# Kernel optimization log

Hardware: AMD Instinct MI355X
Metric: run time of the kernel (lower is better)

The kernel has to match this reference:

```python
import jax, jax.numpy as jnp
import numpy as np

B, C_IN, IMG = 4, 1, 256
E, P = 800, 4            # embed_size, patch_size
H, DH, M = 8, 64, 64     # heads, dim_head=heads**2, num_landmarks
N = (IMG // P) ** 2      # 4096 tokens
OUT = 256                # output_size
RESK = 33                # lucidrains residual depthwise conv kernel
BN_EPS = 1e-5
LN_EPS = 1e-5
PINV_ITERS = 6


def setup_inputs() -> dict:
    key = jax.random.key(0)
    ks = iter(jax.random.split(key, 32))
    def nrm(shape, s=0.02):
        return jax.random.normal(next(ks), shape, jnp.float32) * s
    inp = {"x": jax.random.normal(next(ks), (B, C_IN, IMG, IMG), jnp.float32)}
    # conv stack: (in, out, kernel); last conv has stride=P, padding=0
    for i, (ci, co, kk) in enumerate([(C_IN, 64, 3), (64, 128, 3), (128, 256, 3), (256, E, P)]):
        inp[f"w{i}"] = nrm((co, ci, kk, kk), 0.05)
        inp[f"b{i}"] = jnp.zeros((co,), jnp.float32)
        inp[f"g{i}"] = jnp.ones((co,), jnp.float32)    # BN gamma
        inp[f"be{i}"] = jnp.zeros((co,), jnp.float32)  # BN beta
        inp[f"mu{i}"] = nrm((co,), 0.1)                # BN running mean
        inp[f"var{i}"] = jax.random.uniform(next(ks), (co,), jnp.float32, 0.5, 1.5)
    inp["qkv_w"] = nrm((E, 3 * H * DH))      # to_qkv (no bias)
    inp["out_w"] = nrm((H * DH, E))          # to_out linear
    inp["out_b"] = jnp.zeros((E,), jnp.float32)
    inp["res_w"] = nrm((H, 1, RESK, 1), 0.05)  # depthwise residual conv over token dim
    inp["ln_g"] = jnp.ones((E,), jnp.float32)
    inp["ln_b"] = jnp.zeros((E,), jnp.float32)
    inp["head_w"] = nrm((E, OUT * OUT // N))   # Linear(800, 16)
    inp["head_b"] = jnp.zeros((OUT * OUT // N,), jnp.float32)
    return inp


def conv2d(x, w, b, stride, pad):
    y = jax.lax.conv_general_dilated(x, w, (stride, stride), [(pad, pad), (pad, pad)],
                                     dimension_numbers=("NCHW", "OIHW", "NCHW"))
    return y + b[None, :, None, None]


def bn(x, g, be, mu, var):
    s = g * jax.lax.rsqrt(var + BN_EPS)  # eval-mode BatchNorm
    return x * s[None, :, None, None] + (be - mu * s)[None, :, None, None]


def moore_penrose_pinv(a, iters=PINV_ITERS):
    I = jnp.eye(a.shape[-1], dtype=a.dtype)
    z = jnp.swapaxes(a, -1, -2) / (jnp.max(jnp.abs(a).sum(-1)) * jnp.max(jnp.abs(a).sum(-2)))
    for _ in range(iters):
        az = a @ z
        z = 0.25 * z @ (13.0 * I - az @ (15.0 * I - az @ (7.0 * I - az)))
    return z


def reference(x, w0, b0, g0, be0, mu0, var0, w1, b1, g1, be1, mu1, var1,
              w2, b2, g2, be2, mu2, var2, w3, b3, g3, be3, mu3, var3,
              qkv_w, out_w, out_b, res_w, ln_g, ln_b, head_w, head_b):
    # ---- PatchEmbedConv ----
    h = x
    blocks = [(w0, b0, g0, be0, mu0, var0, 1, 1), (w1, b1, g1, be1, mu1, var1, 1, 1),
              (w2, b2, g2, be2, mu2, var2, 1, 1), (w3, b3, g3, be3, mu3, var3, P, 0)]
    for w, b, g, be, mu, var, st, pd in blocks:
        h = jax.nn.relu(bn(conv2d(h, w, b, st, pd), g, be, mu, var))
    tok = h.reshape(B, E, N).transpose(0, 2, 1)  # [B, N, E]

    # ---- NystromAttention (n % m == 0, so no front padding needed) ----
    qkv = tok @ qkv_w  # [B, N, 3*H*DH]
    q, k, v = [t.reshape(B, N, H, DH).transpose(0, 2, 1, 3) for t in jnp.split(qkv, 3, axis=-1)]
    q = q * (DH ** -0.5)
    l = N // M
    q_l = q.reshape(B, H, M, l, DH).mean(3)  # landmark means over consecutive blocks
    k_l = k.reshape(B, H, M, l, DH).mean(3)
    a1 = jax.nn.softmax(jnp.einsum("bhnd,bhmd->bhnm", q, k_l), axis=-1)    # [B,H,N,M]
    a2 = jax.nn.softmax(jnp.einsum("bhmd,bhkd->bhmk", q_l, k_l), axis=-1)  # [B,H,M,M]
    a3 = jax.nn.softmax(jnp.einsum("bhmd,bhnd->bhmn", q_l, k), axis=-1)    # [B,H,M,N]
    out = (a1 @ moore_penrose_pinv(a2)) @ (a3 @ v)  # [B,H,N,DH]
    # residual depthwise conv over the token dim of v (groups = heads)
    res = jax.lax.conv_general_dilated(v, res_w, (1, 1), [(RESK // 2, RESK // 2), (0, 0)],
                                       dimension_numbers=("NCHW", "OIHW", "NCHW"),
                                       feature_group_count=H)
    out = out + res
    out = out.transpose(0, 2, 1, 3).reshape(B, N, H * DH)
    out = out @ out_w + out_b  # [B, N, E]

    # ---- LayerNorm ----
    mu_t = out.mean(-1, keepdims=True)
    var_t = out.var(-1, keepdims=True)
    out = (out - mu_t) * jax.lax.rsqrt(var_t + LN_EPS) * ln_g + ln_b

    # ---- reconstruction head ----
    y = jax.nn.sigmoid(out @ head_w + head_b)  # [B, N, OUT*OUT/N]
    return y.reshape(-1, 1, OUT, OUT)
```

## Files before the change

kernel.cpp:

```cpp
#include <hip/hip_runtime.h>

#define DI __device__ __forceinline__

constexpr float BN_EPS_C = 1e-5f;
constexpr float LN_EPS_C = 1e-5f;

typedef _Float16 half8 __attribute__((ext_vector_type(8)));
typedef float f32x4 __attribute__((ext_vector_type(4)));

constexpr size_t B_H0   = 0;
constexpr size_t B_H1   = 8388608;
constexpr size_t B_H2   = 25165824;
constexpr size_t B_Q    = 25165824;
constexpr size_t B_V    = 58720256;
constexpr size_t B_KT   = 75497472;
constexpr size_t B_ATT  = 92274688;
constexpr size_t B_LNB  = 25165824;
constexpr size_t B_TOK  = 159383552;
constexpr size_t B_WP1  = 185597952;
constexpr size_t B_WP2  = 185745408;
constexpr size_t B_WP3  = 186335232;
constexpr size_t B_QKVT = 192888832;
constexpr size_t B_OWT  = 195346432;
constexpr size_t B_QL   = 196165632;
constexpr size_t B_KL   = 196689920;
constexpr size_t B_KLH  = 197214208;
constexpr size_t B_A2   = 197476352;
constexpr size_t B_W2T  = 198524928;
constexpr size_t B_A3V  = 198787072;
constexpr size_t B_SCAL = 199311360;
constexpr size_t B_HWH  = 199311424;

DI float blockReduceSum(float v) {
  #pragma unroll
  for (int o = 32; o; o >>= 1) v += __shfl_xor(v, o);
  __shared__ float red[4];
  int w = threadIdx.x >> 6;
  __syncthreads();
  if ((threadIdx.x & 63) == 0) red[w] = v;
  __syncthreads();
  return red[0] + red[1] + red[2] + red[3];
}

template <int LP, int RP>
DI void mm16(const float* L, const float* R, int r0, int c0, float reg[4][4]) {
  #pragma unroll
  for (int i = 0; i < 4; ++i)
    #pragma unroll
    for (int j = 0; j < 4; ++j) reg[i][j] = 0.f;
  for (int dd = 0; dd < 64; ++dd) {
    float l[4], r[4];
    #pragma unroll
    for (int i = 0; i < 4; ++i) l[i] = L[(size_t)(r0 + i) * LP + dd];
    #pragma unroll
    for (int j = 0; j < 4; ++j) r[j] = R[(size_t)dd * RP + c0 + j];
    #pragma unroll
    for (int i = 0; i < 4; ++i)
      #pragma unroll
      for (int j = 0; j < 4; ++j) reg[i][j] = fmaf(l[i], r[j], reg[i][j]);
  }
}

__global__ void k_pack_all(
    const float* __restrict__ w1, const float* __restrict__ w2c, const float* __restrict__ w3,
    const float* __restrict__ qkvw, const float* __restrict__ outw, const float* __restrict__ headw,
    _Float16* __restrict__ wp1, _Float16* __restrict__ wp2, _Float16* __restrict__ wp3,
    _Float16* __restrict__ qkvT, _Float16* __restrict__ owT, _Float16* __restrict__ hwh,
    float* __restrict__ scal) {
  size_t i = (size_t)blockIdx.x * 256 + threadIdx.x;
  if (i < 73728) {
    int q = i % 9, ci = (i / 9) % 64, co = i / (9 * 64);
    wp1[((size_t)co * 9 + q) * 64 + ci] = (_Float16)w1[i];
  } else if (i < 368640) {
    size_t j = i - 73728;
    int q = j % 9, ci = (j / 9) % 128, co = j / (9 * 128);
    wp2[((size_t)co * 9 + q) * 128 + ci] = (_Float16)w2c[j];
  } else if (i < 3645440) {
    size_t j = i - 368640;
    int q = j % 16, ci = (j / 16) % 256, co = j / (16 * 256);
    wp3[((size_t)co * 16 + q) * 256 + ci] = (_Float16)w3[j];
  } else if (i < 4874240) {
    size_t j = i - 3645440;
    int n = j % 1536, k = j / 1536;
    qkvT[(size_t)n * 800 + k] = (_Float16)qkvw[j];
  } else if (i < 5283840) {
    size_t j = i - 4874240;
    int n = j % 800, k = j / 800;
    owT[(size_t)n * 512 + k] = (_Float16)outw[j];
  } else if (i < 5296640) {
    size_t j = i - 5283840;
    int n = j % 16, k = j / 16;
    hwh[(size_t)n * 800 + k] = (_Float16)headw[j];
  } else if (i < 5296642) {
    scal[i - 5296640] = 0.f;
  }
}

__global__ __launch_bounds__(256) void k_conv0(
    const float* __restrict__ xb, const float* __restrict__ w0, const float* __restrict__ b0,
    const float* __restrict__ g0, const float* __restrict__ be0, const float* __restrict__ mu0,
    const float* __restrict__ var0, _Float16* __restrict__ h0) {
  const int t = threadIdx.x, co = t & 63, xg = t >> 6;
  const int y = blockIdx.x;
  float wreg[9];
  #pragma unroll
  for (int q = 0; q < 9; ++q) wreg[q] = w0[co * 9 + q];
  float s = g0[co] * rsqrtf(var0[co] + BN_EPS_C);
  float sh = fmaf(b0[co] - mu0[co], s, be0[co]);
  for (int xl = 0; xl < 64; ++xl) {
    int xx = xg * 64 + xl;
    float acc = 0.f;
    #pragma unroll
    for (int dy = 0; dy < 3; ++dy) {
      int yy = y + dy - 1;
      if ((unsigned)yy >= 256u) continue;
      #pragma unroll
      for (int dx = 0; dx < 3; ++dx) {
        int xi = xx + dx - 1;
        if ((unsigned)xi >= 256u) continue;
        acc = fmaf(wreg[dy * 3 + dx], xb[yy * 256 + xi], acc);
      }
    }
    float v = fmaxf(fmaf(acc, s, sh), 0.f);
    h0[((size_t)y * 256 + xx) * 64 + co] = (_Float16)v;
  }
}

template <int CI>
__global__ __launch_bounds__(256) void k_convs(
    const _Float16* __restrict__ in, const _Float16* __restrict__ wp,
    const float* __restrict__ bias, const float* __restrict__ g, const float* __restrict__ be,
    const float* __restrict__ mu, const float* __restrict__ var,
    _Float16* __restrict__ out, int CO, int NCT) {
  __shared__ _Float16 Ab[2][128 * 40];
  __shared__ _Float16 Bb[2][128 * 40];
  constexpr int CPQ = CI / 32;
  constexpr int NCK = 9 * CPQ;
  const int t = threadIdx.x;
  const int bid = blockIdx.x;
  const int xcd = bid & 7, slot = bid >> 3;
  const int pj = slot / NCT, cc = slot % NCT;
  const int p = pj * 8 + xcd;
  const int r0 = p * 128, c0 = cc * 128;

  const int ma = t >> 2, kga = t & 3;
  int ry[2], rx[2];
  #pragma unroll
  for (int s = 0; s < 2; ++s) {
    int r = r0 + ma + s * 64;
    ry[s] = r >> 8;
    rx[s] = r & 255;
  }
  const _Float16* baseB[2];
  #pragma unroll
  for (int s = 0; s < 2; ++s)
    baseB[s] = wp + (size_t)(c0 + ma + s * 64) * 9 * CI + kga * 8;
  const int wo = ma * 40 + kga * 8;

  auto loadA = [&](int s, int ck) -> half8 {
    int q = ck / CPQ, coff = (ck % CPQ) * 32;
    int yy = ry[s] + q / 3 - 1;
    int xx = rx[s] + q % 3 - 1;
    half8 a = {};
    if ((unsigned)yy < 256u && (unsigned)xx < 256u)
      a = *reinterpret_cast<const half8*>(in + ((size_t)yy * 256 + xx) * CI + coff + kga * 8);
    return a;
  };

  {
    half8 a0 = loadA(0, 0), a1 = loadA(1, 0);
    half8 b0v = *reinterpret_cast<const half8*>(baseB[0]);
    half8 b1v = *reinterpret_cast<const half8*>(baseB[1]);
    *reinterpret_cast<half8*>(&Ab[0][wo]) = a0;
    *reinterpret_cast<half8*>(&Ab[0][wo + 2560]) = a1;
    *reinterpret_cast<half8*>(&Bb[0][wo]) = b0v;
    *reinterpret_cast<half8*>(&Bb[0][wo + 2560]) = b1v;
  }
  __syncthreads();

  const int w = t >> 6, lo = t & 15, hi = (t >> 4) & 3;
  const int wm = w >> 1, wn = w & 1;
  const int roA = (wm * 64 + lo) * 40 + 8 * hi;
  const int roB = (wn * 64 + lo) * 40 + 8 * hi;
  f32x4 acc[4][4] = {};

  for (int ck = 0; ck < NCK; ++ck) {
    const int cur = ck & 1;
    const bool more = (ck + 1 < NCK);
    half8 rA0, rA1, rB0, rB1;
    if (more) {
      rA0 = loadA(0, ck + 1);
      rA1 = loadA(1, ck + 1);
      rB0 = *reinterpret_cast<const half8*>(baseB[0] + (ck + 1) * 32);
      rB1 = *reinterpret_cast<const half8*>(baseB[1] + (ck + 1) * 32);
    }
    half8 af[4], bf[4];
    #pragma unroll
    for (int mi = 0; mi < 4; ++mi)
      af[mi] = *reinterpret_cast<const half8*>(&Ab[cur][roA + mi * 640]);
    #pragma unroll
    for (int ni = 0; ni < 4; ++ni)
      bf[ni] = *reinterpret_cast<const half8*>(&Bb[cur][roB + ni * 640]);
    #pragma unroll
    for (int mi = 0; mi < 4; ++mi)
      #pragma unroll
      for (int ni = 0; ni < 4; ++ni)
        acc[mi][ni] = __builtin_amdgcn_mfma_f32_16x16x32_f16(af[mi], bf[ni], acc[mi][ni], 0, 0, 0);
    if (more) {
      *reinterpret_cast<half8*>(&Ab[cur ^ 1][wo]) = rA0;
      *reinterpret_cast<half8*>(&Ab[cur ^ 1][wo + 2560]) = rA1;
      *reinterpret_cast<half8*>(&Bb[cur ^ 1][wo]) = rB0;
      *reinterpret_cast<half8*>(&Bb[cur ^ 1][wo + 2560]) = rB1;
    }
    __syncthreads();
  }

  #pragma unroll
  for (int ni = 0; ni < 4; ++ni) {
    int co = c0 + wn * 64 + ni * 16 + lo;
    float s = g[co] * rsqrtf(var[co] + BN_EPS_C);
    float sh = fmaf(bias[co] - mu[co], s, be[co]);
    #pragma unroll
    for (int mi = 0; mi < 4; ++mi)
      #pragma unroll
      for (int rr = 0; rr < 4; ++rr) {
        int row = r0 + wm * 64 + mi * 16 + hi * 4 + rr;
        float v = fmaxf(fmaf(acc[mi][ni][rr], s, sh), 0.f);
        out[(size_t)row * CO + co] = (_Float16)v;
      }
  }
}

__global__ __launch_bounds__(256) void k_c3(
    const _Float16* __restrict__ h2, const _Float16* __restrict__ wp3,
    const float* __restrict__ b3, const float* __restrict__ g3, const float* __restrict__ be3,
    const float* __restrict__ mu3, const float* __restrict__ var3,
    _Float16* __restrict__ tok) {
  __shared__ _Float16 Abuf[2][128 * 40];
  __shared__ _Float16 Bbuf[2][160 * 40];
  const int t = threadIdx.x;
  const int bid = blockIdx.x;
  const int xcd = bid & 7, slot = bid >> 3;
  const int pj = slot / 5, cc = slot % 5;
  const int p = pj * 8 + xcd;
  const int r0 = p * 128, c0 = cc * 160;
  const int img = r0 >> 12;
  const _Float16* h2i = h2 + (size_t)img * 16777216;

  const int ma = t >> 2, kga = t & 3;
  const _Float16* baseA[2];
  #pragma unroll
  for (int s = 0; s < 2; ++s) {
    int m = ma + s * 64;
    int r = r0 + m;
    int py = (r & 4095) >> 6, px = r & 63;
    baseA[s] = h2i + ((size_t)py * 1024 + px * 4) * 256 + kga * 8;
  }
  const _Float16* baseB[3];
  #pragma unroll
  for (int s = 0; s < 3; ++s) {
    int cb = ma + s * 64;
    baseB[s] = wp3 + (size_t)(c0 + (cb < 160 ? cb : 159)) * 4096 + kga * 8;
  }
  const int wo = ma * 40 + kga * 8;

  const int w = t >> 6, lo = t & 15, hi = (t >> 4) & 3;
  const int wm = w >> 1, wn = w & 1;
  const int roA = (wm * 64 + lo) * 40 + 8 * hi;
  const int roB = (wn * 80 + lo) * 40 + 8 * hi;

  f32x4 acc[4][5] = {};

  {
    half8 a0 = *reinterpret_cast<const half8*>(baseA[0]);
    half8 a1 = *reinterpret_cast<const half8*>(baseA[1]);
    half8 b0v = *reinterpret_cast<const half8*>(baseB[0]);
    half8 b1v = *reinterpret_cast<const half8*>(baseB[1]);
    *reinterpret_cast<half8*>(&Abuf[0][wo]) = a0;
    *reinterpret_cast<half8*>(&Abuf[0][wo + 2560]) = a1;
    *reinterpret_cast<half8*>(&Bbuf[0][wo]) = b0v;
    *reinterpret_cast<half8*>(&Bbuf[0][wo + 2560]) = b1v;
    if (t < 128) {
      half8 b2v = *reinterpret_cast<const half8*>(baseB[2]);
      *reinterpret_cast<half8*>(&Bbuf[0][wo + 5120]) = b2v;
    }
  }
  __syncthreads();

  for (int ck = 0; ck < 128; ++ck) {
    const int cur = ck & 1;
    const bool more = (ck + 1 < 128);
    half8 rA0, rA1, rB0, rB1, rB2;
    if (more) {
      const int kn = (ck + 1) << 5;
      const int q = kn >> 8, qk = kn & 255;
      const int aoff = (q >> 2) * 65536 + (q & 3) * 256 + qk;
      rA0 = *reinterpret_cast<const half8*>(baseA[0] + aoff);
      rA1 = *reinterpret_cast<const half8*>(baseA[1] + aoff);
      rB0 = *reinterpret_cast<const half8*>(baseB[0] + kn);
      rB1 = *reinterpret_cast<const half8*>(baseB[1] + kn);
      if (t < 128) rB2 = *reinterpret_cast<const half8*>(baseB[2] + kn);
    }
    half8 af[4], bf[5];
    #pragma unroll
    for (int mi = 0; mi < 4; ++mi)
      af[mi] = *reinterpret_cast<const half8*>(&Abuf[cur][roA + mi * 640]);
    #pragma unroll
    for (int ni = 0; ni < 5; ++ni)
      bf[ni] = *reinterpret_cast<const half8*>(&Bbuf[cur][roB + ni * 640]);
    #pragma unroll
    for (int mi = 0; mi < 4; ++mi)
      #pragma unroll
      for (int ni = 0; ni < 5; ++ni)
        acc[mi][ni] = __builtin_amdgcn_mfma_f32_16x16x32_f16(af[mi], bf[ni], acc[mi][ni], 0, 0, 0);
    if (more) {
      *reinterpret_cast<half8*>(&Abuf[cur ^ 1][wo]) = rA0;
      *reinterpret_cast<half8*>(&Abuf[cur ^ 1][wo + 2560]) = rA1;
      *reinterpret_cast<half8*>(&Bbuf[cur ^ 1][wo]) = rB0;
      *reinterpret_cast<half8*>(&Bbuf[cur ^ 1][wo + 2560]) = rB1;
      if (t < 128) *reinterpret_cast<half8*>(&Bbuf[cur ^ 1][wo + 5120]) = rB2;
    }
    __syncthreads();
  }

  #pragma unroll
  for (int ni = 0; ni < 5; ++ni) {
    int col = c0 + wn * 80 + ni * 16 + lo;
    float s = g3[col] * rsqrtf(var3[col] + BN_EPS_C);
    float sh = fmaf(b3[col] - mu3[col], s, be3[col]);
    #pragma unroll
    for (int mi = 0; mi < 4; ++mi)
      #pragma unroll
      for (int rr = 0; rr < 4; ++rr) {
        int row = r0 + wm * 64 + mi * 16 + hi * 4 + rr;
        float v = fmaxf(fmaf(acc[mi][ni][rr], s, sh), 0.f);
        tok[(size_t)row * 800 + col] = (_Float16)v;
      }
  }
}

__global__ __launch_bounds__(256) void k_qkv_s(
    const _Float16* __restrict__ tok, const _Float16* __restrict__ qkvT,
    _Float16* __restrict__ qx, _Float16* __restrict__ kTg, _Float16* __restrict__ vx) {
  __shared__ _Float16 Ab[2][128 * 40];
  __shared__ _Float16 Bb[2][128 * 40];
  const int t = threadIdx.x;
  const int bid = blockIdx.x;
  const int xcd = bid & 7, slot = bid >> 3;
  const int pj = slot / 12, cc = slot % 12;
  const int p = pj * 8 + xcd;
  const int r0 = p * 128, c0 = cc * 128;

  const int ma = t >> 2, kga = t & 3;
  const _Float16* baseA[2];
  const _Float16* baseB[2];
  #pragma unroll
  for (int s = 0; s < 2; ++s) {
    baseA[s] = tok + (size_t)(r0 + ma + s * 64) * 800 + kga * 8;
    baseB[s] = qkvT + (size_t)(c0 + ma + s * 64) * 800 + kga * 8;
  }
  const int wo = ma * 40 + kga * 8;

  {
    half8 a0 = *reinterpret_cast<const half8*>(baseA[0]);
    half8 a1 = *reinterpret_cast<const half8*>(baseA[1]);
    half8 b0v = *reinterpret_cast<const half8*>(baseB[0]);
    half8 b1v = *reinterpret_cast<const half8*>(baseB[1]);
    *reinterpret_cast<half8*>(&Ab[0][wo]) = a0;
    *reinterpret_cast<half8*>(&Ab[0][wo + 2560]) = a1;
    *reinterpret_cast<half8*>(&Bb[0][wo]) = b0v;
    *reinterpret_cast<half8*>(&Bb[0][wo + 2560]) = b1v;
  }
  __syncthreads();

  const int w = t >> 6, lo = t & 15, hi = (t >> 4) & 3;
  const int wm = w >> 1, wn = w & 1;
  const int roA = (wm * 64 + lo) * 40 + 8 * hi;
  const int roB = (wn * 64 + lo) * 40 + 8 * hi;
  f32x4 acc[4][4] = {};

  for (int ck = 0; ck < 25; ++ck) {
    const int cur = ck & 1;
    const bool more = (ck + 1 < 25);
    half8 rA0, rA1, rB0, rB1;
    if (more) {
      const int kn = (ck + 1) * 32;
      rA0 = *reinterpret_cast<const half8*>(baseA[0] + kn);
      rA1 = *reinterpret_cast<const half8*>(baseA[1] + kn);
      rB0 = *reinterpret_cast<const half8*>(baseB[0] + kn);
      rB1 = *reinterpret_cast<const half8*>(baseB[1] + kn);
    }
    half8 af[4], bf[4];
    #pragma unroll
    for (int mi = 0; mi < 4; ++mi)
      af[mi] = *reinterpret_cast<const half8*>(&Ab[cur][roA + mi * 640]);
    #pragma unroll
    for (int ni = 0; ni < 4; ++ni)
      bf[ni] = *reinterpret_cast<const half8*>(&Bb[cur][roB + ni * 640]);
    #pragma unroll
    for (int mi = 0; mi < 4; ++mi)
      #pragma unroll
      for (int ni = 0; ni < 4; ++ni)
        acc[mi][ni] = __builtin_amdgcn_mfma_f32_16x16x32_f16(af[mi], bf[ni], acc[mi][ni], 0, 0, 0);
    if (more) {
      *reinterpret_cast<half8*>(&Ab[cur ^ 1][wo]) = rA0;
      *reinterpret_cast<half8*>(&Ab[cur ^ 1][wo + 2560]) = rA1;
      *reinterpret_cast<half8*>(&Bb[cur ^ 1][wo]) = rB0;
      *reinterpret_cast<half8*>(&Bb[cur ^ 1][wo + 2560]) = rB1;
    }
    __syncthreads();
  }

  const int seg = cc >> 2;
  if (seg == 1) {
    #pragma unroll
    for (int ni = 0; ni < 4; ++ni) {
      int cseg = (cc & 3) * 128 + wn * 64 + ni * 16 + lo;
      int h = cseg >> 6, d = cseg & 63;
      #pragma unroll
      for (int mi = 0; mi < 4; ++mi)
        #pragma unroll
        for (int rr = 0; rr < 4; ++rr) {
          int row = r0 + wm * 64 + mi * 16 + hi * 4 + rr;
          int b = row >> 12, nn = row & 4095;
          kTg[((size_t)(b * 8 + h) * 64 + d) * 4096 + nn] = (_Float16)acc[mi][ni][rr];
        }
    }
  } else {
    const float scale = (seg == 0) ? 0.125f : 1.0f;
    _Float16* dst = (seg == 0) ? qx : vx;
    #pragma unroll
    for (int ni = 0; ni < 4; ++ni) {
      int cseg = (cc & 3) * 128 + wn * 64 + ni * 16 + lo;
      int h = cseg >> 6, d = cseg & 63;
      #pragma unroll
      for (int mi = 0; mi < 4; ++mi)
        #pragma unroll
        for (int rr = 0; rr < 4; ++rr) {
          int row = r0 + wm * 64 + mi * 16 + hi * 4 + rr;
          int b = row >> 12, nn = row & 4095;
          dst[((size_t)(b * 8 + h) * 4096 + nn) * 64 + d] = (_Float16)(acc[mi][ni][rr] * scale);
        }
    }
  }
}

__global__ __launch_bounds__(256) void k_op_s(
    const _Float16* __restrict__ attb, const _Float16* __restrict__ owT,
    const float* __restrict__ ob, _Float16* __restrict__ lnb) {
  __shared__ _Float16 Abuf[2][128 * 40];
  __shared__ _Float16 Bbuf[2][160 * 40];
  const int t = threadIdx.x;
  const int bid = blockIdx.x;
  const int xcd = bid & 7, slot = bid >> 3;
  const int pj = slot / 5, cc = slot % 5;
  const int p = pj * 8 + xcd;
  const int r0 = p * 128, c0 = cc * 160;

  const int ma = t >> 2, kga = t & 3;
  const _Float16* baseA[2];
  #pragma unroll
  for (int s = 0; s < 2; ++s)
    baseA[s] = attb + (size_t)(r0 + ma + s * 64) * 512 + kga * 8;
  const _Float16* baseB[3];
  #pragma unroll
  for (int s = 0; s < 3; ++s) {
    int cb = ma + s * 64;
    baseB[s] = owT + (size_t)(c0 + (cb < 160 ? cb : 159)) * 512 + kga * 8;
  }
  const int wo = ma * 40 + kga * 8;

  const int w = t >> 6, lo = t & 15, hi = (t >> 4) & 3;
  const int wm = w >> 1, wn = w & 1;
  const int roA = (wm * 64 + lo) * 40 + 8 * hi;
  const int roB = (wn * 80 + lo) * 40 + 8 * hi;

  f32x4 acc[4][5] = {};

  {
    half8 a0 = *reinterpret_cast<const half8*>(baseA[0]);
    half8 a1 = *reinterpret_cast<const half8*>(baseA[1]);
    half8 b0v = *reinterpret_cast<const half8*>(baseB[0]);
    half8 b1v = *reinterpret_cast<const half8*>(baseB[1]);
    *reinterpret_cast<half8*>(&Abuf[0][wo]) = a0;
    *reinterpret_cast<half8*>(&Abuf[0][wo + 2560]) = a1;
    *reinterpret_cast<half8*>(&Bbuf[0][wo]) = b0v;
    *reinterpret_cast<half8*>(&Bbuf[0][wo + 2560]) = b1v;
    if (t < 128) {
      half8 b2v = *reinterpret_cast<const half8*>(baseB[2]);
      *reinterpret_cast<half8*>(&Bbuf[0][wo + 5120]) = b2v;
    }
  }
  __syncthreads();

  for (int ck = 0; ck < 16; ++ck) {
    const int cur = ck & 1;
    const bool more = (ck + 1 < 16);
    half8 rA0, rA1, rB0, rB1, rB2;
    if (more) {
      const int kn = (ck + 1) << 5;
      rA0 = *reinterpret_cast<const half8*>(baseA[0] + kn);
      rA1 = *reinterpret_cast<const half8*>(baseA[1] + kn);
      rB0 = *reinterpret_cast<const half8*>(baseB[0] + kn);
      rB1 = *reinterpret_cast<const half8*>(baseB[1] + kn);
      if (t < 128) rB2 = *reinterpret_cast<const half8*>(baseB[2] + kn);
    }
    half8 af[4], bf[5];
    #pragma unroll
    for (int mi = 0; mi < 4; ++mi)
      af[mi] = *reinterpret_cast<const half8*>(&Abuf[cur][roA + mi * 640]);
    #pragma unroll
    for (int ni = 0; ni < 5; ++ni)
      bf[ni] = *reinterpret_cast<const half8*>(&Bbuf[cur][roB + ni * 640]);
    #pragma unroll
    for (int mi = 0; mi < 4; ++mi)
      #pragma unroll
      for (int ni = 0; ni < 5; ++ni)
        acc[mi][ni] = __builtin_amdgcn_mfma_f32_16x16x32_f16(af[mi], bf[ni], acc[mi][ni], 0, 0, 0);
    if (more) {
      *reinterpret_cast<half8*>(&Abuf[cur ^ 1][wo]) = rA0;
      *reinterpret_cast<half8*>(&Abuf[cur ^ 1][wo + 2560]) = rA1;
      *reinterpret_cast<half8*>(&Bbuf[cur ^ 1][wo]) = rB0;
      *reinterpret_cast<half8*>(&Bbuf[cur ^ 1][wo + 2560]) = rB1;
      if (t < 128) *reinterpret_cast<half8*>(&Bbuf[cur ^ 1][wo + 5120]) = rB2;
    }
    __syncthreads();
  }

  #pragma unroll
  for (int ni = 0; ni < 5; ++ni) {
    int col = c0 + wn * 80 + ni * 16 + lo;
    float bv = ob[col];
    #pragma unroll
    for (int mi = 0; mi < 4; ++mi)
      #pragma unroll
      for (int rr = 0; rr < 4; ++rr) {
        int row = r0 + wm * 64 + mi * 16 + hi * 4 + rr;
        lnb[(size_t)row * 800 + col] = (_Float16)(acc[mi][ni][rr] + bv);
      }
  }
}

__global__ __launch_bounds__(64) void k_landmark(
    const _Float16* __restrict__ qx, const _Float16* __restrict__ kT,
    float* __restrict__ ql, float* __restrict__ kl, _Float16* __restrict__ klh) {
  const int d = threadIdx.x;
  const int m = blockIdx.x, bh = blockIdx.y;
  const _Float16* qp = qx + ((size_t)bh * 4096 + m * 64) * 64 + d;
  const _Float16* kp = kT + ((size_t)bh * 64 + d) * 4096 + m * 64;
  float sq = 0.f, sk = 0.f;
  #pragma unroll 8
  for (int j = 0; j < 64; ++j) sq += (float)qp[(size_t)j * 64];
  #pragma unroll
  for (int j = 0; j < 64; j += 8) {
    half8 kv = *reinterpret_cast<const half8*>(kp + j);
    #pragma unroll
    for (int u = 0; u < 8; ++u) sk += (float)kv[u];
  }
  sq *= (1.f / 64.f);
  sk *= (1.f / 64.f);
  ql[((size_t)bh * 64 + m) * 64 + d] = sq;
  kl[((size_t)bh * 64 + m) * 64 + d] = sk;
  klh[((size_t)bh * 64 + m) * 64 + d] = (_Float16)sk;
}

__global__ __launch_bounds__(64) void k_a2(
    const float* __restrict__ ql, const float* __restrict__ kl,
    float* __restrict__ a2, float* __restrict__ scal) {
  __shared__ float sp[64 * 65];
  const int bh = blockIdx.x, t = threadIdx.x;
  const float* qr = ql + ((size_t)bh * 64 + t) * 64;
  const float* kb = kl + (size_t)bh * 4096;
  float mx = -1e30f;
  for (int c = 0; c < 64; ++c) {
    float acc = 0.f;
    #pragma unroll 8
    for (int dd = 0; dd < 64; ++dd) acc = fmaf(qr[dd], kb[c * 64 + dd], acc);
    sp[t * 65 + c] = acc;
    mx = fmaxf(mx, acc);
  }
  float sum = 0.f;
  for (int c = 0; c < 64; ++c) {
    float e = expf(sp[t * 65 + c] - mx);
    sp[t * 65 + c] = e;
    sum += e;
  }
  float inv = 1.f / sum;
  float rs = 0.f;
  for (int c = 0; c < 64; ++c) {
    float p = sp[t * 65 + c] * inv;
    sp[t * 65 + c] = p;
    a2[(size_t)bh * 4096 + t * 64 + c] = p;
    rs += p;
  }
  atomicMax(reinterpret_cast<int*>(scal), __float_as_int(rs));
  __syncthreads();
  float cs = 0.f;
  for (int r = 0; r < 64; ++r) cs += sp[r * 65 + t];
  atomicMax(reinterpret_cast<int*>(scal) + 1, __float_as_int(cs));
}

__global__ __launch_bounds__(256) void k_a3v(
    const float* __restrict__ ql, const _Float16* __restrict__ kT,
    const _Float16* __restrict__ vx, float* __restrict__ a3v) {
  __shared__ float sq[64];
  __shared__ float sP[4096];
  __shared__ float red[4];
  __shared__ float red2[4][64];
  const int t = threadIdx.x;
  const int m = blockIdx.x, bh = blockIdx.y;
  if (t < 64) sq[t] = ql[((size_t)bh * 64 + m) * 64 + t];
  __syncthreads();
  const _Float16* kb = kT + (size_t)bh * 262144;
  float sc[16];
  #pragma unroll
  for (int i = 0; i < 16; ++i) sc[i] = 0.f;
  for (int dd = 0; dd < 64; ++dd) {
    float qv = sq[dd];
    const _Float16* kr = kb + (size_t)dd * 4096 + t;
    #pragma unroll
    for (int i = 0; i < 16; ++i) sc[i] = fmaf(qv, (float)kr[i * 256], sc[i]);
  }
  float mx = sc[0];
  #pragma unroll
  for (int i = 1; i < 16; ++i) mx = fmaxf(mx, sc[i]);
  #pragma unroll
  for (int o = 32; o; o >>= 1) mx = fmaxf(mx, __shfl_xor(mx, o));
  if ((t & 63) == 0) red[t >> 6] = mx;
  __syncthreads();
  mx = fmaxf(fmaxf(red[0], red[1]), fmaxf(red[2], red[3]));
  __syncthreads();
  float sum = 0.f;
  #pragma unroll
  for (int i = 0; i < 16; ++i) {
    sc[i] = expf(sc[i] - mx);
    sum += sc[i];
  }
  #pragma unroll
  for (int o = 32; o; o >>= 1) sum += __shfl_xor(sum, o);
  if ((t & 63) == 0) red[t >> 6] = sum;
  __syncthreads();
  sum = red[0] + red[1] + red[2] + red[3];
  float inv = 1.f / sum;
  #pragma unroll
  for (int i = 0; i < 16; ++i) sP[t + i * 256] = sc[i] * inv;
  __syncthreads();
  const int d = t & 63, seg = t >> 6;
  const _Float16* vb = vx + (size_t)bh * 262144;
  float acc = 0.f;
  for (int n = seg * 1024; n < seg * 1024 + 1024; ++n)
    acc = fmaf(sP[n], (float)vb[(size_t)n * 64 + d], acc);
  red2[seg][d] = acc;
  __syncthreads();
  if (seg == 0)
    a3v[((size_t)bh * 64 + m) * 64 + d] = red2[0][d] + red2[1][d] + red2[2][d] + red2[3][d];
}

__global__ __launch_bounds__(256) void k_pinv(
    const float* __restrict__ a2g, const float* __restrict__ scal,
    const float* __restrict__ a3vg, _Float16* __restrict__ w2t) {
  __shared__ float z[64 * 65];
  __shared__ float az[64 * 65];
  __shared__ float tb[64 * 65];
  const int bh = blockIdx.x, t = threadIdx.x;
  const int r0 = (t >> 4) << 2, c0 = (t & 15) << 2;
  const float* ag = a2g + (size_t)bh * 4096;
  const float denom = 1.f / (scal[0] * scal[1]);
  #pragma unroll
  for (int i = 0; i < 4; ++i)
    #pragma unroll
    for (int j = 0; j < 4; ++j)
      z[(r0 + i) * 65 + c0 + j] = ag[(c0 + j) * 64 + r0 + i] * denom;
  __syncthreads();
  float reg[4][4], val[4][4];
  for (int it = 0; it < 6; ++it) {
    mm16<64, 65>(ag, z, r0, c0, reg);
    #pragma unroll
    for (int i = 0; i < 4; ++i)
      #pragma unroll
      for (int j = 0; j < 4; ++j) az[(r0 + i) * 65 + c0 + j] = reg[i][j];
    __syncthreads();
    mm16<65, 65>(az, az, r0, c0, reg);
    #pragma unroll
    for (int i = 0; i < 4; ++i)
      #pragma unroll
      for (int j = 0; j < 4; ++j)
        tb[(r0 + i) * 65 + c0 + j] = 7.f * az[(r0 + i) * 65 + c0 + j] - reg[i][j];
    __syncthreads();
    mm16<65, 65>(az, tb, r0, c0, reg);
    #pragma unroll
    for (int i = 0; i < 4; ++i)
      #pragma unroll
      for (int j = 0; j < 4; ++j)
        val[i][j] = 15.f * az[(r0 + i) * 65 + c0 + j] - reg[i][j];
    __syncthreads();
    #pragma unroll
    for (int i = 0; i < 4; ++i)
      #pragma unroll
      for (int j = 0; j < 4; ++j) tb[(r0 + i) * 65 + c0 + j] = val[i][j];
    __syncthreads();
    mm16<65, 65>(z, tb, r0, c0, reg);
    #pragma unroll
    for (int i = 0; i < 4; ++i)
      #pragma unroll
      for (int j = 0; j < 4; ++j)
        val[i][j] = 0.25f * (13.f * z[(r0 + i) * 65 + c0 + j] - reg[i][j]);
    __syncthreads();
    #pragma unroll
    for (int i = 0; i < 4; ++i)
      #pragma unroll
      for (int j = 0; j < 4; ++j) z[(r0 + i) * 65 + c0 + j] = val[i][j];
    __syncthreads();
  }
  mm16<65, 64>(z, a3vg + (size_t)bh * 4096, r0, c0, reg);
  #pragma unroll
  for (int i = 0; i < 4; ++i)
    #pragma unroll
    for (int j = 0; j < 4; ++j)
      w2t[(size_t)bh * 4096 + (c0 + j) * 64 + (r0 + i)] = (_Float16)reg[i][j];
}

__global__ __launch_bounds__(256) void k_combine_m(
    const _Float16* __restrict__ qx, const _Float16* __restrict__ klh,
    const _Float16* __restrict__ w2t, const _Float16* __restrict__ vx,
    const float* __restrict__ rw, _Float16* __restrict__ att) {
  __shared__ _Float16 sP[64 * 72];
  __shared__ _Float16 sVT[64 * 104];
  __shared__ _Float16 sT[64 * 104];
  __shared__ float sR[33];
  const int t = threadIdx.x, w = t >> 6, lo = t & 15, hi = (t >> 4) & 3;
  const int n0 = blockIdx.x * 64;
  const int h = blockIdx.y, b = blockIdx.z, bh = b * 8 + h;
  if (t < 33) sR[t] = rw[h * 33 + t];
  __syncthreads();
  const _Float16* vb = vx + (size_t)bh * 262144;
  #pragma unroll
  for (int u = 0; u < 24; ++u) {
    int e = t + u * 256;
    int r = e >> 6, d = e & 63;
    int nn = n0 - 16 + r;
    sVT[d * 104 + r] = ((unsigned)nn < 4096u) ? vb[(size_t)nn * 64 + d] : (_Float16)0.f;
  }
  #pragma unroll
  for (int u = 0; u < 24; ++u) {
    int e = t + u * 256;
    int r = e % 96, i = e / 96;
    int j = r - i;
    sT[i * 104 + r] = (j >= 0 && j < 33) ? (_Float16)sR[j] : (_Float16)0.f;
  }
  f32x4 sa[4] = {};
  const _Float16* qp = qx + ((size_t)bh * 4096 + n0 + w * 16 + lo) * 64 + 8 * hi;
  const _Float16* klp = klh + (size_t)bh * 4096;
  #pragma unroll
  for (int c = 0; c < 2; ++c) {
    half8 a = *reinterpret_cast<const half8*>(qp + 32 * c);
    #pragma unroll
    for (int ct = 0; ct < 4; ++ct) {
      half8 bf = *reinterpret_cast<const half8*>(klp + (size_t)(ct * 16 + lo) * 64 + 8 * hi + 32 * c);
      sa[ct] = __builtin_amdgcn_mfma_f32_16x16x32_f16(a, bf, sa[ct], 0, 0, 0);
    }
  }
  #pragma unroll
  for (int r = 0; r < 4; ++r) {
    float mx = fmaxf(fmaxf(sa[0][r], sa[1][r]), fmaxf(sa[2][r], sa[3][r]));
    #pragma unroll
    for (int o = 8; o; o >>= 1) mx = fmaxf(mx, __shfl_xor(mx, o));
    float e0 = expf(sa[0][r] - mx), e1 = expf(sa[1][r] - mx);
    float e2 = expf(sa[2][r] - mx), e3 = expf(sa[3][r] - mx);
    float sm = e0 + e1 + e2 + e3;
    #pragma unroll
    for (int o = 8; o; o >>= 1) sm += __shfl_xor(sm, o);
    float inv = 1.f / sm;
    int row = w * 16 + hi * 4 + r;
    sP[row * 72 + lo] = (_Float16)(e0 * inv);
    sP[row * 72 + 16 + lo] = (_Float16)(e1 * inv);
    sP[row * 72 + 32 + lo] = (_Float16)(e2 * inv);
    sP[row * 72 + 48 + lo] = (_Float16)(e3 * inv);
  }
  __syncthreads();
  f32x4 ao[4] = {};
  const _Float16* w2p = w2t + (size_t)bh * 4096;
  #pragma unroll
  for (int c = 0; c < 2; ++c) {
    half8 a = *reinterpret_cast<const half8*>(&sP[(w * 16 + lo) * 72 + 8 * hi + 32 * c]);
    #pragma unroll
    for (int ct = 0; ct < 4; ++ct) {
      half8 bf = *reinterpret_cast<const half8*>(w2p + (size_t)(ct * 16 + lo) * 64 + 8 * hi + 32 * c);
      ao[ct] = __builtin_amdgcn_mfma_f32_16x16x32_f16(a, bf, ao[ct], 0, 0, 0);
    }
  }
  #pragma unroll
  for (int c = 0; c < 3; ++c) {
    half8 a = *reinterpret_cast<const half8*>(&sT[(w * 16 + lo) * 104 + 8 * hi + 32 * c]);
    #pragma unroll
    for (int ct = 0; ct < 4; ++ct) {
      half8 bf = *reinterpret_cast<const half8*>(&sVT[(ct * 16 + lo) * 104 + 8 * hi + 32 * c]);
      ao[ct] = __builtin_amdgcn_mfma_f32_16x16x32_f16(a, bf, ao[ct], 0, 0, 0);
    }
  }
  _Float16* ab = att + ((size_t)b * 4096) * 512 + (size_t)h * 64;
  #pragma unroll
  for (int ct = 0; ct < 4; ++ct)
    #pragma unroll
    for (int r = 0; r < 4; ++r) {
      int n = n0 + w * 16 + hi * 4 + r;
      ab[(size_t)n * 512 + ct * 16 + lo] = (_Float16)ao[ct][r];
    }
}

__global__ __launch_bounds__(256) void k_ln16(
    _Float16* __restrict__ buf, const float* __restrict__ g, const float* __restrict__ bb) {
  const int t = threadIdx.x;
  _Float16* p = buf + (size_t)blockIdx.x * 800;
  float x0 = (float)p[t], x1 = (float)p[t + 256], x2 = (float)p[t + 512];
  float x3 = (t < 32) ? (float)p[t + 768] : 0.f;
  float s = blockReduceSum(x0 + x1 + x2 + x3);
  float mean = s * (1.f / 800.f);
  float d0 = x0 - mean, d1 = x1 - mean, d2 = x2 - mean;
  float d3 = (t < 32) ? x3 - mean : 0.f;
  float s2 = blockReduceSum(d0 * d0 + d1 * d1 + d2 * d2 + d3 * d3);
  float rstd = rsqrtf(s2 * (1.f / 800.f) + LN_EPS_C);
  p[t] = (_Float16)(d0 * rstd * g[t] + bb[t]);
  p[t + 256] = (_Float16)(d1 * rstd * g[t + 256] + bb[t + 256]);
  p[t + 512] = (_Float16)(d2 * rstd * g[t + 512] + bb[t + 512]);
  if (t < 32) p[t + 768] = (_Float16)(d3 * rstd * g[t + 768] + bb[t + 768]);
}

__global__ __launch_bounds__(256) void k_head_m(
    const _Float16* __restrict__ ln, const _Float16* __restrict__ hwh,
    const float* __restrict__ hb, float* __restrict__ out) {
  const int t = threadIdx.x, w = t >> 6, lo = t & 15, hi = (t >> 4) & 3;
  const int row0 = blockIdx.x * 64 + w * 16;
  const _Float16* ap = ln + (size_t)(row0 + lo) * 800 + 8 * hi;
  const _Float16* bp = hwh + (size_t)lo * 800 + 8 * hi;
  f32x4 acc = {};
  #pragma unroll 5
  for (int k = 0; k < 800; k += 32) {
    half8 a = *reinterpret_cast<const half8*>(ap + k);
    half8 b = *reinterpret_cast<const half8*>(bp + k);
    acc = __builtin_amdgcn_mfma_f32_16x16x32_f16(a, b, acc, 0, 0, 0);
  }
  float bv = hb[lo];
  #pragma unroll
  for (int r = 0; r < 4; ++r) {
    int row = row0 + hi * 4 + r;
    out[(size_t)row * 16 + lo] = 1.f / (1.f + expf(-(acc[r] + bv)));
  }
}

extern "C" void kernel_launch(void* const* d_in, const int* in_sizes, int n_in,
                              void* d_out, int out_size, void* d_ws, size_t ws_size,
                              hipStream_t stream) {
  (void)in_sizes; (void)n_in; (void)out_size; (void)ws_size;
  const float* x     = (const float*)d_in[0];
  const float* w0    = (const float*)d_in[1];
  const float* b0    = (const float*)d_in[2];
  const float* g0    = (const float*)d_in[3];
  const float* be0   = (const float*)d_in[4];
  const float* mu0   = (const float*)d_in[5];
  const float* var0  = (const float*)d_in[6];
  const float* w1    = (const float*)d_in[7];
  const float* b1    = (const float*)d_in[8];
  const float* g1    = (const float*)d_in[9];
  const float* be1   = (const float*)d_in[10];
  const float* mu1   = (const float*)d_in[11];
  const float* var1  = (const float*)d_in[12];
  const float* w2c   = (const float*)d_in[13];
  const float* b2    = (const float*)d_in[14];
  const float* g2    = (const float*)d_in[15];
  const float* be2   = (const float*)d_in[16];
  const float* mu2   = (const float*)d_in[17];
  const float* var2  = (const float*)d_in[18];
  const float* w3    = (const float*)d_in[19];
  const float* b3    = (const float*)d_in[20];
  const float* g3    = (const float*)d_in[21];
  const float* be3   = (const float*)d_in[22];
  const float* mu3   = (const float*)d_in[23];
  const float* var3  = (const float*)d_in[24];
  const float* qkvw  = (const float*)d_in[25];
  const float* outw  = (const float*)d_in[26];
  const float* outbv = (const float*)d_in[27];
  const float* resw  = (const float*)d_in[28];
  const float* lng   = (const float*)d_in[29];
  const float* lnbv  = (const float*)d_in[30];
  const float* headw = (const float*)d_in[31];
  const float* headb = (const float*)d_in[32];

  char* wsb = (char*)d_ws;
  _Float16* h0   = (_Float16*)(wsb + B_H0);
  _Float16* h1   = (_Float16*)(wsb + B_H1);
  _Float16* h2   = (_Float16*)(wsb + B_H2);
  _Float16* qb   = (_Float16*)(wsb + B_Q);
  _Float16* vb   = (_Float16*)(wsb + B_V);
  _Float16* kT   = (_Float16*)(wsb + B_KT);
  _Float16* tok  = (_Float16*)(wsb + B_TOK);
  _Float16* attb = (_Float16*)(wsb + B_ATT);
  _Float16* wp1  = (_Float16*)(wsb + B_WP1);
  _Float16* wp2  = (_Float16*)(wsb + B_WP2);
  _Float16* wp3  = (_Float16*)(wsb + B_WP3);
  _Float16* qkvT = (_Float16*)(wsb + B_QKVT);
  _Float16* owT  = (_Float16*)(wsb + B_OWT);
  _Float16* klh  = (_Float16*)(wsb + B_KLH);
  _Float16* w2t  = (_Float16*)(wsb + B_W2T);
  _Float16* hwh  = (_Float16*)(wsb + B_HWH);
  _Float16* lnb16 = (_Float16*)(wsb + B_LNB);
  float* ql   = (float*)(wsb + B_QL);
  float* kl   = (float*)(wsb + B_KL);
  float* a2   = (float*)(wsb + B_A2);
  float* a3v  = (float*)(wsb + B_A3V);
  float* scal = (float*)(wsb + B_SCAL);

  k_pack_all<<<dim3(20691), 256, 0, stream>>>(
      w1, w2c, w3, qkvw, outw, headw, wp1, wp2, wp3, qkvT, owT, hwh, scal);

  for (int img = 0; img < 4; ++img) {
    k_conv0<<<dim3(256), 256, 0, stream>>>(
        x + (size_t)img * 65536, w0, b0, g0, be0, mu0, var0, h0);
    k_convs<64><<<dim3(512), 256, 0, stream>>>(
        h0, wp1, b1, g1, be1, mu1, var1, h1, 128, 1);
    k_convs<128><<<dim3(1024), 256, 0, stream>>>(
        h1, wp2, b2, g2, be2, mu2, var2, h2 + (size_t)img * 16777216, 256, 2);
  }
  k_c3<<<dim3(640), 256, 0, stream>>>(h2, wp3, b3, g3, be3, mu3, var3, tok);
  k_qkv_s<<<dim3(1536), 256, 0, stream>>>(tok, qkvT, qb, kT, vb);
  k_landmark<<<dim3(64, 32), 64, 0, stream>>>(qb, kT, ql, kl, klh);
  k_a2<<<dim3(32), 64, 0, stream>>>(ql, kl, a2, scal);
  k_a3v<<<dim3(64, 32), 256, 0, stream>>>(ql, kT, vb, a3v);
  k_pinv<<<dim3(32), 256, 0, stream>>>(a2, scal, a3v, w2t);
  k_combine_m<<<dim3(64, 8, 4), 256, 0, stream>>>(qb, klh, w2t, vb, resw, attb);
  k_op_s<<<dim3(640), 256, 0, stream>>>(attb, owT, outbv, lnb16);
  k_ln16<<<dim3(16384), 256, 0, stream>>>(lnb16, lng, lnbv);
  k_head_m<<<dim3(256), 256, 0, stream>>>(lnb16, hwh, headb, (float*)d_out);
}
```

Measured before the change: 1.153 ms.

## Fuse landmark means into QKV epilogue, vectorize pinv matmuls and a3 loads

Landmark means for q and k are now computed in the QKV GEMM epilogue via register sums and wave shuffles, which removes the separate k_landmark kernel and its re-read of q and k. The pinv inner matmul switches to float4 LDS loads with rows padded to 68, and the a3 kernel reads contiguous half8 chunks of kT per thread, with the matching sP index change. Landmark means are now summed in fp32 before the fp16 rounding of q and k, so values may differ slightly.

```diff
diff --git a/kernel.cpp b/kernel.cpp
--- a/kernel.cpp
+++ b/kernel.cpp
@@ -43,21 +43,27 @@
 }
 
 template <int LP, int RP>
-DI void mm16(const float* L, const float* R, int r0, int c0, float reg[4][4]) {
+DI void mm16v(const float* L, const float* R, int r0, int c0, float reg[4][4]) {
   #pragma unroll
   for (int i = 0; i < 4; ++i)
     #pragma unroll
     for (int j = 0; j < 4; ++j) reg[i][j] = 0.f;
-  for (int dd = 0; dd < 64; ++dd) {
-    float l[4], r[4];
-    #pragma unroll
-    for (int i = 0; i < 4; ++i) l[i] = L[(size_t)(r0 + i) * LP + dd];
-    #pragma unroll
-    for (int j = 0; j < 4; ++j) r[j] = R[(size_t)dd * RP + c0 + j];
+  #pragma unroll 4
+  for (int dd = 0; dd < 64; dd += 4) {
+    f32x4 l[4], rv[4];
     #pragma unroll
     for (int i = 0; i < 4; ++i)
-      #pragma unroll
-      for (int j = 0; j < 4; ++j) reg[i][j] = fmaf(l[i], r[j], reg[i][j]);
+      l[i] = *reinterpret_cast<const f32x4*>(&L[(size_t)(r0 + i) * LP + dd]);
+    #pragma unroll
+    for (int u = 0; u < 4; ++u)
+      rv[u] = *reinterpret_cast<const f32x4*>(&R[(size_t)(dd + u) * RP + c0]);
+    #pragma unroll
+    for (int i = 0; i < 4; ++i)
+      #pragma unroll
+      for (int u = 0; u < 4; ++u)
+        #pragma unroll
+        for (int j = 0; j < 4; ++j)
+          reg[i][j] = fmaf(l[i][u], rv[u][j], reg[i][j]);
   }
 }
 
@@ -341,7 +347,8 @@
 
 __global__ __launch_bounds__(256) void k_qkv_s(
     const _Float16* __restrict__ tok, const _Float16* __restrict__ qkvT,
-    _Float16* __restrict__ qx, _Float16* __restrict__ kTg, _Float16* __restrict__ vx) {
+    _Float16* __restrict__ qx, _Float16* __restrict__ kTg, _Float16* __restrict__ vx,
+    float* __restrict__ ql, float* __restrict__ kl, _Float16* __restrict__ klh) {
   __shared__ _Float16 Ab[2][128 * 40];
   __shared__ _Float16 Bb[2][128 * 40];
   const int t = threadIdx.x;
@@ -412,6 +419,8 @@
   }
 
   const int seg = cc >> 2;
+  const int b = r0 >> 12;
+  const int m = ((r0 & 4095) >> 6) + wm;
   if (seg == 1) {
     #pragma unroll
     for (int ni = 0; ni < 4; ++ni) {
@@ -422,7 +431,7 @@
         #pragma unroll
         for (int rr = 0; rr < 4; ++rr) {
           int row = r0 + wm * 64 + mi * 16 + hi * 4 + rr;
-          int b = row >> 12, nn = row & 4095;
+          int nn = row & 4095;
           kTg[((size_t)(b * 8 + h) * 64 + d) * 4096 + nn] = (_Float16)acc[mi][ni][rr];
         }
     }
@@ -438,9 +447,34 @@
         #pragma unroll
         for (int rr = 0; rr < 4; ++rr) {
           int row = r0 + wm * 64 + mi * 16 + hi * 4 + rr;
-          int b = row >> 12, nn = row & 4095;
+          int nn = row & 4095;
           dst[((size_t)(b * 8 + h) * 4096 + nn) * 64 + d] = (_Float16)(acc[mi][ni][rr] * scale);
         }
+    }
+  }
+  if (seg <= 1) {
+    const float lscale = ((seg == 0) ? 0.125f : 1.0f) * (1.f / 64.f);
+    #pragma unroll
+    for (int ni = 0; ni < 4; ++ni) {
+      float sum = 0.f;
+      #pragma unroll
+      for (int mi = 0; mi < 4; ++mi)
+        #pragma unroll
+        for (int rr = 0; rr < 4; ++rr) sum += acc[mi][ni][rr];
+      sum += __shfl_xor(sum, 16);
+      sum += __shfl_xor(sum, 32);
+      if (hi == 0) {
+        int cseg = (cc & 3) * 128 + wn * 64 + ni * 16 + lo;
+        int h = cseg >> 6, d = cseg & 63;
+        int bh = b * 8 + h;
+        float lm = sum * lscale;
+        if (seg == 0) {
+          ql[((size_t)bh * 64 + m) * 64 + d] = lm;
+        } else {
+          kl[((size_t)bh * 64 + m) * 64 + d] = lm;
+          klh[((size_t)bh * 64 + m) * 64 + d] = (_Float16)lm;
+        }
+      }
     }
   }
 }
@@ -539,29 +573,6 @@
         lnb[(size_t)row * 800 + col] = (_Float16)(acc[mi][ni][rr] + bv);
       }
   }
-}
-
-__global__ __launch_bounds__(64) void k_landmark(
-    const _Float16* __restrict__ qx, const _Float16* __restrict__ kT,
-    float* __restrict__ ql, float* __restrict__ kl, _Float16* __restrict__ klh) {
-  const int d = threadIdx.x;
-  const int m = blockIdx.x, bh = blockIdx.y;
-  const _Float16* qp = qx + ((size_t)bh * 4096 + m * 64) * 64 + d;
-  const _Float16* kp = kT + ((size_t)bh * 64 + d) * 4096 + m * 64;
-  float sq = 0.f, sk = 0.f;
-  #pragma unroll 8
-  for (int j = 0; j < 64; ++j) sq += (float)qp[(size_t)j * 64];
-  #pragma unroll
-  for (int j = 0; j < 64; j += 8) {
-    half8 kv = *reinterpret_cast<const half8*>(kp + j);
-    #pragma unroll
-    for (int u = 0; u < 8; ++u) sk += (float)kv[u];
-  }
-  sq *= (1.f / 64.f);
-  sk *= (1.f / 64.f);
-  ql[((size_t)bh * 64 + m) * 64 + d] = sq;
-  kl[((size_t)bh * 64 + m) * 64 + d] = sk;
-  klh[((size_t)bh * 64 + m) * 64 + d] = (_Float16)sk;
 }
 
 __global__ __launch_bounds__(64) void k_a2(
@@ -617,9 +628,12 @@
   for (int i = 0; i < 16; ++i) sc[i] = 0.f;
   for (int dd = 0; dd < 64; ++dd) {
     float qv = sq[dd];
-    const _Float16* kr = kb + (size_t)dd * 4096 + t;
-    #pragma unroll
-    for (int i = 0; i < 16; ++i) sc[i] = fmaf(qv, (float)kr[i * 256], sc[i]);
+    const half8* kr = reinterpret_cast<const half8*>(kb + (size_t)dd * 4096 + t * 16);
+    half8 k0 = kr[0], k1 = kr[1];
+    #pragma unroll
+    for (int i = 0; i < 8; ++i) sc[i] = fmaf(qv, (float)k0[i], sc[i]);
+    #pragma unroll
+    for (int i = 0; i < 8; ++i) sc[8 + i] = fmaf(qv, (float)k1[i], sc[8 + i]);
   }
   float mx = sc[0];
   #pragma unroll
@@ -643,7 +657,7 @@
   sum = red[0] + red[1] + red[2] + red[3];
   float inv = 1.f / sum;
   #pragma unroll
-  for (int i = 0; i < 16; ++i) sP[t + i * 256] = sc[i] * inv;
+  for (int i = 0; i < 16; ++i) sP[t * 16 + i] = sc[i] * inv;
   __syncthreads();
   const int d = t & 63, seg = t >> 6;
   const _Float16* vb = vx + (size_t)bh * 262144;
@@ -659,9 +673,9 @@
 __global__ __launch_bounds__(256) void k_pinv(
     const float* __restrict__ a2g, const float* __restrict__ scal,
     const float* __restrict__ a3vg, _Float16* __restrict__ w2t) {
-  __shared__ float z[64 * 65];
-  __shared__ float az[64 * 65];
-  __shared__ float tb[64 * 65];
+  __shared__ float z[64 * 68];
+  __shared__ float az[64 * 68];
+  __shared__ float tb[64 * 68];
   const int bh = blockIdx.x, t = threadIdx.x;
   const int r0 = (t >> 4) << 2, c0 = (t & 15) << 2;
   const float* ag = a2g + (size_t)bh * 4096;
@@ -670,49 +684,49 @@
   for (int i = 0; i < 4; ++i)
     #pragma unroll
     for (int j = 0; j < 4; ++j)
-      z[(r0 + i) * 65 + c0 + j] = ag[(c0 + j) * 64 + r0 + i] * denom;
+      z[(r0 + i) * 68 + c0 + j] = ag[(c0 + j) * 64 + r0 + i] * denom;
   __syncthreads();
   float reg[4][4], val[4][4];
   for (int it = 0; it < 6; ++it) {
-    mm16<64, 65>(ag, z, r0, c0, reg);
+    mm16v<64, 68>(ag, z, r0, c0, reg);
     #pragma unroll
     for (int i = 0; i < 4; ++i)
       #pragma unroll
-      for (int j = 0; j < 4; ++j) az[(r0 + i) * 65 + c0 + j] = reg[i][j];
+      for (int j = 0; j < 4; ++j) az[(r0 + i) * 68 + c0 + j] = reg[i][j];
     __syncthreads();
-    mm16<65, 65>(az, az, r0, c0, reg);
+    mm16v<68, 68>(az, az, r0, c0, reg);
     #pragma unroll
     for (int i = 0; i < 4; ++i)
       #pragma unroll
       for (int j = 0; j < 4; ++j)
-        tb[(r0 + i) * 65 + c0 + j] = 7.f * az[(r0 + i) * 65 + c0 + j] - reg[i][j];
+        tb[(r0 + i) * 68 + c0 + j] = 7.f * az[(r0 + i) * 68 + c0 + j] - reg[i][j];
     __syncthreads();
-    mm16<65, 65>(az, tb, r0, c0, reg);
+    mm16v<68, 68>(az, tb, r0, c0, reg);
     #pragma unroll
     for (int i = 0; i < 4; ++i)
       #pragma unroll
       for (int j = 0; j < 4; ++j)
-        val[i][j] = 15.f * az[(r0 + i) * 65 + c0 + j] - reg[i][j];
+        val[i][j] = 15.f * az[(r0 + i) * 68 + c0 + j] - reg[i][j];
     __syncthreads();
     #pragma unroll
     for (int i = 0; i < 4; ++i)
       #pragma unroll
-      for (int j = 0; j < 4; ++j) tb[(r0 + i) * 65 + c0 + j] = val[i][j];
+      for (int j = 0; j < 4; ++j) tb[(r0 + i) * 68 + c0 + j] = val[i][j];
     __syncthreads();
-    mm16<65, 65>(z, tb, r0, c0, reg);
+    mm16v<68, 68>(z, tb, r0, c0, reg);
     #pragma unroll
     for (int i = 0; i < 4; ++i)
       #pragma unroll
       for (int j = 0; j < 4; ++j)
-        val[i][j] = 0.25f * (13.f * z[(r0 + i) * 65 + c0 + j] - reg[i][j]);
+        val[i][j] = 0.25f * (13.f * z[(r0 + i) * 68 + c0 + j] - reg[i][j]);
     __syncthreads();
     #pragma unroll
     for (int i = 0; i < 4; ++i)
       #pragma unroll
-      for (int j = 0; j < 4; ++j) z[(r0 + i) * 65 + c0 + j] = val[i][j];
+      for (int j = 0; j < 4; ++j) z[(r0 + i) * 68 + c0 + j] = val[i][j];
     __syncthreads();
   }
-  mm16<65, 64>(z, a3vg + (size_t)bh * 4096, r0, c0, reg);
+  mm16v<68, 64>(z, a3vg + (size_t)bh * 4096, r0, c0, reg);
   #pragma unroll
   for (int i = 0; i < 4; ++i)
     #pragma unroll
@@ -922,8 +936,7 @@
         h1, wp2, b2, g2, be2, mu2, var2, h2 + (size_t)img * 16777216, 256, 2);
   }
   k_c3<<<dim3(640), 256, 0, stream>>>(h2, wp3, b3, g3, be3, mu3, var3, tok);
-  k_qkv_s<<<dim3(1536), 256, 0, stream>>>(tok, qkvT, qb, kT, vb);
-  k_landmark<<<dim3(64, 32), 64, 0, stream>>>(qb, kT, ql, kl, klh);
+  k_qkv_s<<<dim3(1536), 256, 0, stream>>>(tok, qkvT, qb, kT, vb, ql, kl, klh);
   k_a2<<<dim3(32), 64, 0, stream>>>(ql, kl, a2, scal);
   k_a3v<<<dim3(64, 32), 256, 0, stream>>>(ql, kT, vb, a3v);
   k_pinv<<<dim3(32), 256, 0, stream>>>(a2, scal, a3v, w2t);
```

After: 1.114 ms. 1.03x faster.
